# Kernel optimization log

Measured on AMD Instinct MI355X. Metric: run time of the kernel, lower is better.

## Reference

```python
import jax, jax.numpy as jnp
import numpy as np

LPB = 0.03   # lower_probability_bound
LEB = 0.2    # lower_entropy_bound
UEB = 0.5    # upper_entropy_bound
BETA = 1.0
N, K, S, D = 8192, 1000, 8, 1024


def setup_inputs() -> dict:
    key = jax.random.key(0)
    k1, k2, k3 = jax.random.split(key, 3)
    x = jax.random.normal(k1, (N, D), dtype=jnp.float32)
    # per-sample logit temperature so entropies spread across the gating band
    base = jax.random.normal(k2, (N, K), dtype=jnp.float32)
    scales = jax.random.uniform(k3, (N, 1), dtype=jnp.float32, minval=1.0, maxval=15.0)
    text_logits = base * scales
    memory = jnp.zeros((K, S, D), dtype=jnp.float32)
    # init_entropy(prop_max=1): -log(1/K) = log(K)
    memory_entropy = jnp.full((K, S), jnp.log(jnp.float32(K)), dtype=jnp.float32)
    memory_state = jnp.zeros((K, S), dtype=bool)
    return {"x": x, "text_logits": text_logits, "memory": memory,
            "memory_entropy": memory_entropy, "memory_state": memory_state}


def _update_memory(memory, memory_entropy, memory_state, x, text_logits):
    """Sequential entropy-gated scatter update (order-dependent, as in torch loop)."""
    def step(carry, inp):
        mem, ent, st = carry
        xi, li = inp                      # xi: [D], li: [K]
        p = jax.nn.softmax(li)
        lab = jnp.argmax(li)
        H = -jnp.sum(jnp.log(p + 1e-6) * p)  # shannon entropy
        row = ent[lab]                    # [S] entropies of this class's slots
        cond = (p[lab] > LPB) & (H > LEB) & (H < UEB) & jnp.any(H < row)
        idx = jnp.argmax(row)             # evict highest-entropy slot
        mem = mem.at[lab, idx].set(jnp.where(cond, xi, mem[lab, idx]))
        ent = ent.at[lab, idx].set(jnp.where(cond, H, ent[lab, idx]))
        st = st.at[lab, idx].set(jnp.where(cond, True, st[lab, idx]))
        return (mem, ent, st), cond

    (mem, ent, st), selected = jax.lax.scan(
        step, (memory, memory_entropy, memory_state), (x, text_logits))
    return mem, ent, st, selected


def reference(x, text_logits, memory, memory_entropy, memory_state):
    mem, ent, st, selected = _update_memory(memory, memory_entropy, memory_state, x, text_logits)
    # get_logits: A_ = (memory @ x.T).permute(2,0,1) -> [N, K, S]
    A_ = jnp.einsum('ksd,nd->nks', mem, x)
    logits = -jnp.sum(jnp.exp(-BETA * (1.0 - A_)), axis=-1)  # [N, K]
    return logits
```

## Files before the change

### kernel.cpp

```cpp
#include <hip/hip_runtime.h>
#include <hip/hip_bf16.h>
#include <math.h>

#define NN 8192
#define KK 1000
#define SS 8
#define DD 1024
#define RR (KK * SS)
#define RRP 8192

typedef __bf16 bf16x8 __attribute__((ext_vector_type(8)));
typedef float f32x4 __attribute__((ext_vector_type(4)));
typedef unsigned short ushort_t;
typedef ushort_t ushort8 __attribute__((ext_vector_type(8)));

static __device__ __forceinline__ ushort_t f2bf(float f) {
  unsigned u = __float_as_uint(f);
  unsigned r = (u + 0x7FFFu + ((u >> 16) & 1u)) >> 16;
  return (ushort_t)r;
}

#define GLD16(gsrc, ldst)                                                     \
  __builtin_amdgcn_global_load_lds(                                           \
      (const __attribute__((address_space(1))) unsigned int*)(gsrc),          \
      (__attribute__((address_space(3))) unsigned int*)(ldst), 16, 0, 0)

#define SBAR() asm volatile("s_barrier" ::: "memory")
#define WAITVM(n) asm volatile("s_waitcnt vmcnt(" #n ")" ::: "memory")

__global__ __launch_bounds__(256) void stats_kernel(
    const float* __restrict__ tl, int2* __restrict__ cand) {
  __shared__ float sv[KK];
  __shared__ float redv[256];
  __shared__ int   redi[256];
  const int n = blockIdx.x;
  const int t = threadIdx.x;
  const float* row = tl + (size_t)n * KK;
  for (int j = t; j < KK; j += 256) sv[j] = row[j];
  __syncthreads();

  float bv = -INFINITY; int bi = KK;
  for (int j = t; j < KK; j += 256) { float v = sv[j]; if (v > bv) { bv = v; bi = j; } }
  redv[t] = bv; redi[t] = bi;
  __syncthreads();
  for (int off = 128; off > 0; off >>= 1) {
    if (t < off) {
      float ov = redv[t + off]; int oi = redi[t + off];
      if (ov > redv[t] || (ov == redv[t] && oi < redi[t])) { redv[t] = ov; redi[t] = oi; }
    }
    __syncthreads();
  }
  const float m = redv[0];
  const int lab = redi[0];
  __syncthreads();

  float z = 0.f;
  for (int j = t; j < KK; j += 256) z += expf(sv[j] - m);
  redv[t] = z;
  __syncthreads();
  for (int off = 128; off > 0; off >>= 1) {
    if (t < off) redv[t] += redv[t + off];
    __syncthreads();
  }
  const float Z = redv[0];
  __syncthreads();

  float h = 0.f;
  for (int j = t; j < KK; j += 256) {
    float p = expf(sv[j] - m) / Z;
    h -= p * logf(p + 1e-6f);
  }
  redv[t] = h;
  __syncthreads();
  for (int off = 128; off > 0; off >>= 1) {
    if (t < off) redv[t] += redv[t + off];
    __syncthreads();
  }
  if (t == 0) {
    const float H = redv[0];
    const float plab = 1.0f / Z;
    const bool c = (plab > 0.03f) && (H > 0.2f) && (H < 0.5f);
    cand[n] = make_int2(c ? lab : -1, __float_as_int(H));
  }
}

__global__ __launch_bounds__(256) void select_kernel(
    const int2* __restrict__ cand, const float* __restrict__ ment,
    int* __restrict__ sel) {
  const int w = threadIdx.x >> 6;
  const int l = threadIdx.x & 63;
  const int k = blockIdx.x * 4 + w;
  if (k >= KK) return;

  float ent[SS]; int idx[SS];
  #pragma unroll
  for (int s = 0; s < SS; ++s) { ent[s] = ment[k * SS + s]; idx[s] = -1; }

  for (int base = 0; base < NN; base += 64) {
    const int2 c = cand[base + l];
    unsigned long long msk = __ballot(c.x == k);
    while (msk) {
      const int src = __ffsll((long long)msk) - 1;
      msk &= msk - 1;
      const float H = __shfl(__int_as_float(c.y), src);
      float mx = ent[0]; int mi = 0;
      #pragma unroll
      for (int s = 1; s < SS; ++s) if (ent[s] > mx) { mx = ent[s]; mi = s; }
      if (H < mx) { ent[mi] = H; idx[mi] = base + src; }
    }
  }
  if (l == 0) {
    #pragma unroll
    for (int s = 0; s < SS; ++s) sel[k * SS + s] = idx[s];
  }
}

__global__ __launch_bounds__(128) void xconv_kernel(
    const float* __restrict__ x, ushort_t* __restrict__ xb) {
  const int r = blockIdx.x;
  const int t = threadIdx.x;
  const float4 a = *(const float4*)(x + (size_t)r * DD + t * 8);
  const float4 b = *(const float4*)(x + (size_t)r * DD + t * 8 + 4);
  ushort8 o;
  o[0] = f2bf(a.x); o[1] = f2bf(a.y); o[2] = f2bf(a.z); o[3] = f2bf(a.w);
  o[4] = f2bf(b.x); o[5] = f2bf(b.y); o[6] = f2bf(b.z); o[7] = f2bf(b.w);
  *(ushort8*)(xb + (size_t)r * DD + t * 8) = o;
}

__global__ __launch_bounds__(128) void gather_kernel(
    const float* __restrict__ x, const float* __restrict__ mem,
    const int* __restrict__ sel, ushort_t* __restrict__ Bb) {
  const int r = blockIdx.x;
  const int t = threadIdx.x;
  if (r >= RR) {
    ushort8 z = (ushort8)0;
    *(ushort8*)(Bb + (size_t)r * DD + t * 8) = z;
    return;
  }
  const int sl = sel[r];
  const float* src = (sl >= 0) ? (x + (size_t)sl * DD) : (mem + (size_t)r * DD);
  const float4 a = *(const float4*)(src + t * 8);
  const float4 b = *(const float4*)(src + t * 8 + 4);
  ushort8 o;
  o[0] = f2bf(a.x); o[1] = f2bf(a.y); o[2] = f2bf(a.z); o[3] = f2bf(a.w);
  o[4] = f2bf(b.x); o[5] = f2bf(b.y); o[6] = f2bf(b.z); o[7] = f2bf(b.w);
  *(ushort8*)(Bb + (size_t)r * DD + t * 8) = o;
}

#define BKT 32
#define NT (DD / BKT)

__global__ __launch_bounds__(512, 2) void logits_kernel(
    const ushort_t* __restrict__ xb, const ushort_t* __restrict__ Bb,
    float* __restrict__ out) {
  __shared__ ushort_t lds[4 * 16384];
  const int t = threadIdx.x;
  const int w = t >> 6;
  const int l = t & 63;
  const int wm = w >> 2;
  const int wn = w & 3;
  const int n0 = blockIdx.x * 256;
  const int r0 = blockIdx.y * 256;

  const int srow = w * 16 + (l >> 2);
  const int schunkh = (((l & 3) ^ ((l >> 3) & 3)) << 3);
  const ushort_t* gA0 = xb + (size_t)(n0 + srow) * DD + schunkh;
  const ushort_t* gA1 = xb + (size_t)(n0 + srow + 128) * DD + schunkh;
  const ushort_t* gB0 = Bb + (size_t)(r0 + srow) * DD + schunkh;
  const ushort_t* gB1 = Bb + (size_t)(r0 + srow + 128) * DD + schunkh;

#define STAGE_A(T, p) do {                                                    \
    GLD16(gA0 + (size_t)(T) * BKT, lds + (p) * 16384 + w * 512);              \
    GLD16(gA1 + (size_t)(T) * BKT, lds + (p) * 16384 + 4096 + w * 512);       \
  } while (0)
#define STAGE_B(T, p) do {                                                    \
    GLD16(gB0 + (size_t)(T) * BKT, lds + (p) * 16384 + 8192 + w * 512);       \
    GLD16(gB1 + (size_t)(T) * BKT, lds + (p) * 16384 + 12288 + w * 512);      \
  } while (0)

  const int lr = l & 15;
  const int ch = l >> 4;
  const int swz = ((ch ^ ((lr >> 1) & 3)) << 3);
  const int Aoff = (wm * 128 + lr) * 32 + swz;
  const int Boff = 8192 + (wn * 64 + lr) * 32 + swz;

  f32x4 acc[8][4];
  #pragma unroll
  for (int mi = 0; mi < 8; ++mi)
    #pragma unroll
    for (int ni = 0; ni < 4; ++ni) acc[mi][ni] = (f32x4){0.f, 0.f, 0.f, 0.f};

  STAGE_A(0, 0); STAGE_B(0, 0);
  STAGE_A(1, 1); STAGE_B(1, 1);
  STAGE_A(2, 2); STAGE_B(2, 2);
  WAITVM(8);
  SBAR();

  #pragma unroll 4
  for (int T = 0; T < NT; ++T) {
    const int p = T & 3;
    const ushort_t* buf = lds + p * 16384;
    bf16x8 af[4], bfr[4];

    #pragma unroll
    for (int mi = 0; mi < 4; ++mi)
      af[mi] = *(const bf16x8*)(buf + Aoff + mi * 512);
    #pragma unroll
    for (int ni = 0; ni < 4; ++ni)
      bfr[ni] = *(const bf16x8*)(buf + Boff + ni * 512);
    if (T + 3 < NT) STAGE_A(T + 3, (T + 3) & 3);
    SBAR();
    __builtin_amdgcn_s_setprio(1);
    #pragma unroll
    for (int mi = 0; mi < 4; ++mi)
      #pragma unroll
      for (int ni = 0; ni < 4; ++ni)
        acc[mi][ni] = __builtin_amdgcn_mfma_f32_16x16x32_bf16(
            af[mi], bfr[ni], acc[mi][ni], 0, 0, 0);
    __builtin_amdgcn_s_setprio(0);
    SBAR();

    #pragma unroll
    for (int mi = 0; mi < 4; ++mi)
      af[mi] = *(const bf16x8*)(buf + Aoff + 2048 + mi * 512);
    if (T + 3 < NT) STAGE_B(T + 3, (T + 3) & 3);
    SBAR();
    __builtin_amdgcn_s_setprio(1);
    #pragma unroll
    for (int mi = 0; mi < 4; ++mi)
      #pragma unroll
      for (int ni = 0; ni < 4; ++ni)
        acc[mi + 4][ni] = __builtin_amdgcn_mfma_f32_16x16x32_bf16(
            af[mi], bfr[ni], acc[mi + 4][ni], 0, 0, 0);
    __builtin_amdgcn_s_setprio(0);
    if (T < NT - 3) { WAITVM(8); }
    else if (T == NT - 3) { WAITVM(4); }
    else if (T == NT - 2) { WAITVM(0); }
    SBAR();
  }

  const int rbase = n0 + wm * 128 + ((l >> 4) * 4);
  #pragma unroll
  for (int mi = 0; mi < 8; ++mi) {
    #pragma unroll
    for (int ni = 0; ni < 4; ++ni) {
      const int colbase = r0 + wn * 64 + ni * 16 + (l & 15);
      const int cls = colbase >> 3;
      #pragma unroll
      for (int rg = 0; rg < 4; ++rg) {
        float e = __expf(acc[mi][ni][rg] - 1.0f);
        e += __shfl_xor(e, 1);
        e += __shfl_xor(e, 2);
        e += __shfl_xor(e, 4);
        if ((l & 7) == 0 && cls < KK) {
          out[(size_t)(rbase + mi * 16 + rg) * KK + cls] = -fminf(e, 3.0e38f);
        }
      }
    }
  }
}

extern "C" void kernel_launch(void* const* d_in, const int* in_sizes, int n_in,
                              void* d_out, int out_size, void* d_ws, size_t ws_size,
                              hipStream_t stream) {
  const float* x    = (const float*)d_in[0];
  const float* tl   = (const float*)d_in[1];
  const float* mem  = (const float*)d_in[2];
  const float* ment = (const float*)d_in[3];
  float* out = (float*)d_out;

  char* ws = (char*)d_ws;
  int2*     cand = (int2*)ws;
  int*      sel  = (int*)(ws + NN * 8);
  ushort_t* Bb   = (ushort_t*)(ws + (1 << 20));
  ushort_t* xb   = (ushort_t*)(ws + (1 << 20) + (size_t)RRP * DD * 2);

  hipLaunchKernelGGL(stats_kernel, dim3(NN), dim3(256), 0, stream, tl, cand);
  hipLaunchKernelGGL(select_kernel, dim3(250), dim3(256), 0, stream, cand, ment, sel);
  hipLaunchKernelGGL(xconv_kernel, dim3(NN), dim3(128), 0, stream, x, xb);
  hipLaunchKernelGGL(gather_kernel, dim3(RRP), dim3(128), 0, stream, x, mem, sel, Bb);
  hipLaunchKernelGGL(logits_kernel, dim3(32, 32), dim3(512), 0, stream, xb, Bb, out);
}
```

Baseline: 241.3 us.

## Merge conversion and gather kernels; restructure GEMM loop with fewer barriers

Folds the x-to-bf16 conversion and the memory gather into one launch, removing a kernel launch and its tail. In the logits GEMM, each K-step now issues both A and B prefetches up front, loads all A and B fragments from LDS at once, and runs all 32 MFMAs back to back, dropping three of the four barriers per iteration. This needs more registers for the extra A fragments. The prefetch into buffer (T+3)&3 is issued without a barrier after the previous iteration's reads of that buffer, which relies on the end-of-loop barrier for ordering.

```diff
diff --git a/kernel.cpp b/kernel.cpp
--- a/kernel.cpp
+++ b/kernel.cpp
@@ -115,36 +115,33 @@
   }
 }
 
-__global__ __launch_bounds__(128) void xconv_kernel(
-    const float* __restrict__ x, ushort_t* __restrict__ xb) {
+__global__ __launch_bounds__(128) void convgather_kernel(
+    const float* __restrict__ x, const float* __restrict__ mem,
+    const int* __restrict__ sel, ushort_t* __restrict__ xb,
+    ushort_t* __restrict__ Bb) {
   const int r = blockIdx.x;
   const int t = threadIdx.x;
-  const float4 a = *(const float4*)(x + (size_t)r * DD + t * 8);
-  const float4 b = *(const float4*)(x + (size_t)r * DD + t * 8 + 4);
-  ushort8 o;
-  o[0] = f2bf(a.x); o[1] = f2bf(a.y); o[2] = f2bf(a.z); o[3] = f2bf(a.w);
-  o[4] = f2bf(b.x); o[5] = f2bf(b.y); o[6] = f2bf(b.z); o[7] = f2bf(b.w);
-  *(ushort8*)(xb + (size_t)r * DD + t * 8) = o;
-}
-
-__global__ __launch_bounds__(128) void gather_kernel(
-    const float* __restrict__ x, const float* __restrict__ mem,
-    const int* __restrict__ sel, ushort_t* __restrict__ Bb) {
-  const int r = blockIdx.x;
-  const int t = threadIdx.x;
-  if (r >= RR) {
-    ushort8 z = (ushort8)0;
-    *(ushort8*)(Bb + (size_t)r * DD + t * 8) = z;
-    return;
-  }
-  const int sl = sel[r];
-  const float* src = (sl >= 0) ? (x + (size_t)sl * DD) : (mem + (size_t)r * DD);
+  const float* src;
+  ushort_t* dst;
+  if (r < NN) {
+    src = x + (size_t)r * DD;
+    dst = xb + (size_t)r * DD;
+  } else {
+    const int rr = r - NN;
+    dst = Bb + (size_t)rr * DD;
+    if (rr >= RR) {
+      *(ushort8*)(dst + t * 8) = (ushort8)0;
+      return;
+    }
+    const int sl = sel[rr];
+    src = (sl >= 0) ? (x + (size_t)sl * DD) : (mem + (size_t)rr * DD);
+  }
   const float4 a = *(const float4*)(src + t * 8);
   const float4 b = *(const float4*)(src + t * 8 + 4);
   ushort8 o;
   o[0] = f2bf(a.x); o[1] = f2bf(a.y); o[2] = f2bf(a.z); o[3] = f2bf(a.w);
   o[4] = f2bf(b.x); o[5] = f2bf(b.y); o[6] = f2bf(b.z); o[7] = f2bf(b.w);
-  *(ushort8*)(Bb + (size_t)r * DD + t * 8) = o;
+  *(ushort8*)(dst + t * 8) = o;
 }
 
 #define BKT 32
@@ -200,39 +197,35 @@
   for (int T = 0; T < NT; ++T) {
     const int p = T & 3;
     const ushort_t* buf = lds + p * 16384;
-    bf16x8 af[4], bfr[4];
-
-    #pragma unroll
-    for (int mi = 0; mi < 4; ++mi)
-      af[mi] = *(const bf16x8*)(buf + Aoff + mi * 512);
+    bf16x8 af0[4], af1[4], bfr[4];
+
+    if (T + 3 < NT) { STAGE_A(T + 3, (T + 3) & 3); STAGE_B(T + 3, (T + 3) & 3); }
+
+    #pragma unroll
+    for (int mi = 0; mi < 4; ++mi)
+      af0[mi] = *(const bf16x8*)(buf + Aoff + mi * 512);
     #pragma unroll
     for (int ni = 0; ni < 4; ++ni)
       bfr[ni] = *(const bf16x8*)(buf + Boff + ni * 512);
-    if (T + 3 < NT) STAGE_A(T + 3, (T + 3) & 3);
-    SBAR();
+    #pragma unroll
+    for (int mi = 0; mi < 4; ++mi)
+      af1[mi] = *(const bf16x8*)(buf + Aoff + 2048 + mi * 512);
+
     __builtin_amdgcn_s_setprio(1);
     #pragma unroll
     for (int mi = 0; mi < 4; ++mi)
       #pragma unroll
       for (int ni = 0; ni < 4; ++ni)
         acc[mi][ni] = __builtin_amdgcn_mfma_f32_16x16x32_bf16(
-            af[mi], bfr[ni], acc[mi][ni], 0, 0, 0);
-    __builtin_amdgcn_s_setprio(0);
-    SBAR();
-
-    #pragma unroll
-    for (int mi = 0; mi < 4; ++mi)
-      af[mi] = *(const bf16x8*)(buf + Aoff + 2048 + mi * 512);
-    if (T + 3 < NT) STAGE_B(T + 3, (T + 3) & 3);
-    SBAR();
-    __builtin_amdgcn_s_setprio(1);
+            af0[mi], bfr[ni], acc[mi][ni], 0, 0, 0);
     #pragma unroll
     for (int mi = 0; mi < 4; ++mi)
       #pragma unroll
       for (int ni = 0; ni < 4; ++ni)
         acc[mi + 4][ni] = __builtin_amdgcn_mfma_f32_16x16x32_bf16(
-            af[mi], bfr[ni], acc[mi + 4][ni], 0, 0, 0);
+            af1[mi], bfr[ni], acc[mi + 4][ni], 0, 0, 0);
     __builtin_amdgcn_s_setprio(0);
+
     if (T < NT - 3) { WAITVM(8); }
     else if (T == NT - 3) { WAITVM(4); }
     else if (T == NT - 2) { WAITVM(0); }
@@ -277,7 +270,7 @@
 
   hipLaunchKernelGGL(stats_kernel, dim3(NN), dim3(256), 0, stream, tl, cand);
   hipLaunchKernelGGL(select_kernel, dim3(250), dim3(256), 0, stream, cand, ment, sel);
-  hipLaunchKernelGGL(xconv_kernel, dim3(NN), dim3(128), 0, stream, x, xb);
-  hipLaunchKernelGGL(gather_kernel, dim3(RRP), dim3(128), 0, stream, x, mem, sel, Bb);
+  hipLaunchKernelGGL(convgather_kernel, dim3(NN + RRP), dim3(128), 0, stream,
+                     x, mem, sel, xb, Bb);
   hipLaunchKernelGGL(logits_kernel, dim3(32, 32), dim3(512), 0, stream, xb, Bb, out);
 }
```

After: 237.8 us. About the same (-1.4%).
